# Performance work log

Measured on AMD Instinct MI355X. Metric: run time of the kernel, lower is better.

The kernel has to match this reference:

```python
import jax, jax.numpy as jnp
import numpy as np

B, N, E, F_IN, F_OUT, F_EDGE = 8, 1024, 1536, 64, 64, 32


def _build_graph(seed=0):
    rng = np.random.default_rng(seed)
    src = rng.integers(0, N, size=E)
    off = rng.integers(1, N, size=E)
    dst = (src + off) % N  # guaranteed distinct from src
    inc = np.zeros((N, E), dtype=np.float32)
    inc[src, np.arange(E)] = 1.0
    inc[dst, np.arange(E)] = 1.0
    adj = np.zeros((N, N), dtype=np.float32)
    adj[src, dst] = 1.0
    adj[dst, src] = 1.0
    adj_sl = adj + np.eye(N, dtype=np.float32)
    deg = adj_sl.sum(axis=1)
    dinv = (1.0 / np.sqrt(deg)).astype(np.float32)  # D^{-1/2}, diag
    lap = (dinv[:, None] * adj_sl * dinv[None, :]).astype(np.float32)
    return inc, lap


def setup_inputs() -> dict:
    key = jax.random.key(0)
    k1, k2, k3, k4 = jax.random.split(key, 4)
    inc, lap = _build_graph()
    return {
        "nodes": jax.random.normal(k1, (B, N, F_IN), dtype=jnp.float32),
        "edges": jax.random.normal(k2, (B, E, F_EDGE), dtype=jnp.float32),
        "weight_matrix": jax.random.normal(k3, (F_IN, F_OUT), dtype=jnp.float32),
        "edge_weight_vec": jax.random.normal(k4, (F_EDGE,), dtype=jnp.float32),
        "inc_matrix": jnp.asarray(inc),
        "norm_symm_laplacian": jnp.asarray(lap),
    }


def reference(nodes, edges, weight_matrix, edge_weight_vec, inc_matrix, norm_symm_laplacian):
    # edge feature reduction: [B,E,F_e] @ [F_e] -> [B,E]
    ew = jnp.einsum("bef,f->be", edges, edge_weight_vec)
    # TDT[b,i,j] = sum_e over edges incident to BOTH i and j of ew[b,e].
    # This replaces the original per-(i,j) Python-dict gather loop with one
    # fused contraction over the binary incidence mask.
    incb = (inc_matrix != 0).astype(ew.dtype)           # [N,E]
    tmp = incb[None, :, :] * ew[:, None, :]             # [B,N,E]
    tdt = jnp.einsum("bie,je->bij", tmp, incb)          # [B,N,N]
    a_mat = tdt * norm_symm_laplacian                   # elementwise with D^-1/2(A+I)D^-1/2
    h = nodes @ weight_matrix                           # [B,N,F_out]
    return jnp.einsum("bij,bjf->bif", a_mat, h)         # [B,N,F_out]
```

## Files before the change

### kernel.cpp

```cpp
#include <hip/hip_runtime.h>

#define B_ 8
#define N_ 1024
#define E_ 1536
#define FIN_ 64
#define FOUT_ 64
#define FEDGE_ 32

#define WS_CNT   0
#define WS_ENDS  6144
#define WS_EW    18432
#define WS_DIAG  67584
#define WS_H     100352
#define WS_ZERO_BYTES 100352

__global__ __launch_bounds__(256) void extract_edges(const float* __restrict__ inc,
                                                     int* __restrict__ cnt,
                                                     int* __restrict__ ends) {
    int e = blockIdx.x * 256 + threadIdx.x;
    int i = blockIdx.y;
    if (e >= E_) return;
    if (inc[(size_t)i * E_ + e] != 0.0f) {
        int p = atomicAdd(&cnt[e], 1);
        ends[e * 2 + p] = i;
    }
}

__global__ __launch_bounds__(256) void edge_weights(const float* __restrict__ edges,
                                                    const float* __restrict__ evec,
                                                    const int* __restrict__ ends,
                                                    float* __restrict__ ew,
                                                    float* __restrict__ diag) {
    int t = blockIdx.x * 256 + threadIdx.x;
    if (t >= B_ * E_) return;
    int b = t / E_;
    int e = t - b * E_;
    const float* ep = edges + (size_t)t * FEDGE_;
    float s = 0.0f;
#pragma unroll
    for (int f = 0; f < FEDGE_; ++f) s += ep[f] * evec[f];
    ew[t] = s;
    int u = ends[2 * e];
    int v = ends[2 * e + 1];
    atomicAdd(&diag[b * N_ + u], s);
    atomicAdd(&diag[b * N_ + v], s);
}

__global__ __launch_bounds__(256) void node_transform(const float* __restrict__ nodes,
                                                      const float* __restrict__ W,
                                                      float* __restrict__ h) {
    __shared__ float Wl[FIN_ * FOUT_];
    __shared__ float rows[4 * FIN_];
    int tid = threadIdx.x;
#pragma unroll
    for (int k = tid; k < FIN_ * FOUT_; k += 256) Wl[k] = W[k];
    int row0 = blockIdx.x * 4;
    rows[tid] = nodes[(size_t)row0 * FIN_ + tid];
    __syncthreads();
    int r = tid >> 6;
    int f = tid & 63;
    float acc = 0.0f;
#pragma unroll
    for (int k = 0; k < FIN_; ++k) acc += rows[r * FIN_ + k] * Wl[k * FOUT_ + f];
    h[(size_t)(row0 + r) * FOUT_ + f] = acc;
}

__global__ __launch_bounds__(256) void scatter_edges(const int* __restrict__ ends,
                                                     const float* __restrict__ ew,
                                                     const float* __restrict__ lap,
                                                     const float* __restrict__ h,
                                                     float* __restrict__ out) {
    int wave = (blockIdx.x * 256 + threadIdx.x) >> 6;
    int lane = threadIdx.x & 63;
    if (wave >= B_ * E_) return;
    int b = wave / E_;
    int e = wave - b * E_;
    int u = ends[2 * e];
    int v = ends[2 * e + 1];
    float s = ew[wave] * lap[(size_t)u * N_ + v];
    const float* hb = h + (size_t)b * N_ * FOUT_;
    float* ob = out + (size_t)b * N_ * FOUT_;
    float hv = hb[(size_t)v * FOUT_ + lane];
    float hu = hb[(size_t)u * FOUT_ + lane];
    atomicAdd(&ob[(size_t)u * FOUT_ + lane], s * hv);
    atomicAdd(&ob[(size_t)v * FOUT_ + lane], s * hu);
}

__global__ __launch_bounds__(256) void add_diag(const float* __restrict__ diag,
                                                const float* __restrict__ lap,
                                                const float* __restrict__ h,
                                                float* __restrict__ out) {
    int t = blockIdx.x * 256 + threadIdx.x;
    if (t >= B_ * N_ * FOUT_) return;
    int bi = t >> 6;
    int i = bi & (N_ - 1);
    out[t] += diag[bi] * lap[(size_t)i * N_ + i] * h[t];
}

extern "C" void kernel_launch(void* const* d_in, const int* in_sizes, int n_in,
                              void* d_out, int out_size, void* d_ws, size_t ws_size,
                              hipStream_t stream) {
    const float* nodes = (const float*)d_in[0];
    const float* edges = (const float*)d_in[1];
    const float* W     = (const float*)d_in[2];
    const float* evec  = (const float*)d_in[3];
    const float* inc   = (const float*)d_in[4];
    const float* lap   = (const float*)d_in[5];
    float* out = (float*)d_out;

    char* ws = (char*)d_ws;
    int*   cnt  = (int*)(ws + WS_CNT);
    int*   ends = (int*)(ws + WS_ENDS);
    float* ew   = (float*)(ws + WS_EW);
    float* diag = (float*)(ws + WS_DIAG);
    float* h    = (float*)(ws + WS_H);

    hipMemsetAsync(ws, 0, WS_ZERO_BYTES, stream);
    hipMemsetAsync(d_out, 0, (size_t)out_size * sizeof(float), stream);

    extract_edges<<<dim3((E_ + 255) / 256, N_), 256, 0, stream>>>(inc, cnt, ends);
    node_transform<<<(B_ * N_) / 4, 256, 0, stream>>>(nodes, W, h);
    edge_weights<<<(B_ * E_ + 255) / 256, 256, 0, stream>>>(edges, evec, ends, ew, diag);
    scatter_edges<<<(B_ * E_ * 64) / 256, 256, 0, stream>>>(ends, ew, lap, h, out);
    add_diag<<<(B_ * N_ * FOUT_) / 256, 256, 0, stream>>>(diag, lap, h, out);
}
```

Measured before the change: 97.10 us.

## Fuse prep kernels and fold diagonal term into edge scatter

Merges node transform, incidence extraction and edge-weight reduction into one block-partitioned kernel, and zeroes the output there instead of with a memset. The separate diagonal kernel and its atomics are removed by having each edge add its self-loop contribution s*lap_ii*h_i during the scatter. Edge endpoints are found with atomicMin/atomicMax over a 0xAA-filled buffer using float4 reads. This cuts launch count and passes over the data, at the cost of a few extra lap loads per edge wave.

```diff
diff --git a/kernel.cpp b/kernel.cpp
--- a/kernel.cpp
+++ b/kernel.cpp
@@ -7,94 +7,97 @@
 #define FOUT_ 64
 #define FEDGE_ 32
 
-#define WS_CNT   0
-#define WS_ENDS  6144
-#define WS_EW    18432
-#define WS_DIAG  67584
-#define WS_H     100352
-#define WS_ZERO_BYTES 100352
+#define WS_LO   0
+#define WS_HI   6144
+#define WS_EW   12288
+#define WS_H    61440
 
-__global__ __launch_bounds__(256) void extract_edges(const float* __restrict__ inc,
-                                                     int* __restrict__ cnt,
-                                                     int* __restrict__ ends) {
-    int e = blockIdx.x * 256 + threadIdx.x;
-    int i = blockIdx.y;
-    if (e >= E_) return;
-    if (inc[(size_t)i * E_ + e] != 0.0f) {
-        int p = atomicAdd(&cnt[e], 1);
-        ends[e * 2 + p] = i;
+#define NT_BLOCKS 2048
+#define EX_BLOCKS 1536
+#define EW_BLOCKS 48
+#define K1_BLOCKS (NT_BLOCKS + EX_BLOCKS + EW_BLOCKS)
+
+__global__ __launch_bounds__(256) void fused_prep(
+    const float* __restrict__ nodes,
+    const float* __restrict__ W,
+    const float* __restrict__ inc,
+    const float* __restrict__ edges,
+    const float* __restrict__ evec,
+    unsigned*    __restrict__ ends_lo,
+    int*         __restrict__ ends_hi,
+    float*       __restrict__ ew,
+    float*       __restrict__ h,
+    float*       __restrict__ out)
+{
+    __shared__ float Wl[FIN_ * FOUT_];
+    __shared__ float rows[4 * FIN_];
+    const int blk = blockIdx.x;
+    const int tid = threadIdx.x;
+
+    if (blk < NT_BLOCKS) {
+#pragma unroll
+        for (int k = tid; k < FIN_ * FOUT_; k += 256) Wl[k] = W[k];
+        const int row0 = blk * 4;
+        rows[tid] = nodes[(size_t)row0 * FIN_ + tid];
+        __syncthreads();
+        const int r = tid >> 6;
+        const int f = tid & 63;
+        float acc = 0.0f;
+#pragma unroll
+        for (int k = 0; k < FIN_; ++k) acc += rows[r * FIN_ + k] * Wl[k * FOUT_ + f];
+        const size_t o = (size_t)(row0 + r) * FOUT_ + f;
+        h[o] = acc;
+        out[o] = 0.0f;
+    } else if (blk < NT_BLOCKS + EX_BLOCKS) {
+        const int g = (blk - NT_BLOCKS) * 256 + tid;
+        const int row = g / (E_ / 4);
+        const int q = g - row * (E_ / 4);
+        const float4 c = ((const float4*)inc)[g];
+        const int e0 = q * 4;
+        if (c.x != 0.0f) { atomicMin(&ends_lo[e0 + 0], (unsigned)row); atomicMax(&ends_hi[e0 + 0], row); }
+        if (c.y != 0.0f) { atomicMin(&ends_lo[e0 + 1], (unsigned)row); atomicMax(&ends_hi[e0 + 1], row); }
+        if (c.z != 0.0f) { atomicMin(&ends_lo[e0 + 2], (unsigned)row); atomicMax(&ends_hi[e0 + 2], row); }
+        if (c.w != 0.0f) { atomicMin(&ends_lo[e0 + 3], (unsigned)row); atomicMax(&ends_hi[e0 + 3], row); }
+    } else {
+        const int t = (blk - NT_BLOCKS - EX_BLOCKS) * 256 + tid;
+        const float4* ep = (const float4*)(edges + (size_t)t * FEDGE_);
+        float s = 0.0f;
+#pragma unroll
+        for (int j = 0; j < FEDGE_ / 4; ++j) {
+            const float4 a = ep[j];
+            s += a.x * evec[4 * j + 0] + a.y * evec[4 * j + 1]
+               + a.z * evec[4 * j + 2] + a.w * evec[4 * j + 3];
+        }
+        ew[t] = s;
     }
 }
 
-__global__ __launch_bounds__(256) void edge_weights(const float* __restrict__ edges,
-                                                    const float* __restrict__ evec,
-                                                    const int* __restrict__ ends,
-                                                    float* __restrict__ ew,
-                                                    float* __restrict__ diag) {
-    int t = blockIdx.x * 256 + threadIdx.x;
-    if (t >= B_ * E_) return;
-    int b = t / E_;
-    int e = t - b * E_;
-    const float* ep = edges + (size_t)t * FEDGE_;
-    float s = 0.0f;
-#pragma unroll
-    for (int f = 0; f < FEDGE_; ++f) s += ep[f] * evec[f];
-    ew[t] = s;
-    int u = ends[2 * e];
-    int v = ends[2 * e + 1];
-    atomicAdd(&diag[b * N_ + u], s);
-    atomicAdd(&diag[b * N_ + v], s);
-}
-
-__global__ __launch_bounds__(256) void node_transform(const float* __restrict__ nodes,
-                                                      const float* __restrict__ W,
-                                                      float* __restrict__ h) {
-    __shared__ float Wl[FIN_ * FOUT_];
-    __shared__ float rows[4 * FIN_];
-    int tid = threadIdx.x;
-#pragma unroll
-    for (int k = tid; k < FIN_ * FOUT_; k += 256) Wl[k] = W[k];
-    int row0 = blockIdx.x * 4;
-    rows[tid] = nodes[(size_t)row0 * FIN_ + tid];
-    __syncthreads();
-    int r = tid >> 6;
-    int f = tid & 63;
-    float acc = 0.0f;
-#pragma unroll
-    for (int k = 0; k < FIN_; ++k) acc += rows[r * FIN_ + k] * Wl[k * FOUT_ + f];
-    h[(size_t)(row0 + r) * FOUT_ + f] = acc;
-}
-
-__global__ __launch_bounds__(256) void scatter_edges(const int* __restrict__ ends,
-                                                     const float* __restrict__ ew,
-                                                     const float* __restrict__ lap,
-                                                     const float* __restrict__ h,
-                                                     float* __restrict__ out) {
-    int wave = (blockIdx.x * 256 + threadIdx.x) >> 6;
-    int lane = threadIdx.x & 63;
-    if (wave >= B_ * E_) return;
-    int b = wave / E_;
-    int e = wave - b * E_;
-    int u = ends[2 * e];
-    int v = ends[2 * e + 1];
-    float s = ew[wave] * lap[(size_t)u * N_ + v];
+__global__ __launch_bounds__(256) void scatter_edges(
+    const unsigned* __restrict__ ends_lo,
+    const int*      __restrict__ ends_hi,
+    const float*    __restrict__ ew,
+    const float*    __restrict__ lap,
+    const float*    __restrict__ h,
+    float*          __restrict__ out)
+{
+    const int wid = (blockIdx.x * 256 + threadIdx.x) >> 6;
+    const int lane = threadIdx.x & 63;
+    if (wid >= B_ * E_) return;
+    const int b = wid / E_;
+    const int e = wid - b * E_;
+    const int u = (int)ends_lo[e];
+    const int v = ends_hi[e];
+    const float s = ew[wid];
+    const float* lrow = lap + (size_t)u * N_;
+    const float luv = lrow[v];
+    const float luu = lrow[u];
+    const float lvv = lap[(size_t)v * N_ + v];
     const float* hb = h + (size_t)b * N_ * FOUT_;
     float* ob = out + (size_t)b * N_ * FOUT_;
-    float hv = hb[(size_t)v * FOUT_ + lane];
-    float hu = hb[(size_t)u * FOUT_ + lane];
-    atomicAdd(&ob[(size_t)u * FOUT_ + lane], s * hv);
-    atomicAdd(&ob[(size_t)v * FOUT_ + lane], s * hu);
-}
-
-__global__ __launch_bounds__(256) void add_diag(const float* __restrict__ diag,
-                                                const float* __restrict__ lap,
-                                                const float* __restrict__ h,
-                                                float* __restrict__ out) {
-    int t = blockIdx.x * 256 + threadIdx.x;
-    if (t >= B_ * N_ * FOUT_) return;
-    int bi = t >> 6;
-    int i = bi & (N_ - 1);
-    out[t] += diag[bi] * lap[(size_t)i * N_ + i] * h[t];
+    const float hu = hb[(size_t)u * FOUT_ + lane];
+    const float hv = hb[(size_t)v * FOUT_ + lane];
+    atomicAdd(&ob[(size_t)u * FOUT_ + lane], s * (luv * hv + luu * hu));
+    atomicAdd(&ob[(size_t)v * FOUT_ + lane], s * (luv * hu + lvv * hv));
 }
 
 extern "C" void kernel_launch(void* const* d_in, const int* in_sizes, int n_in,
@@ -109,18 +112,14 @@
     float* out = (float*)d_out;
 
     char* ws = (char*)d_ws;
-    int*   cnt  = (int*)(ws + WS_CNT);
-    int*   ends = (int*)(ws + WS_ENDS);
-    float* ew   = (float*)(ws + WS_EW);
-    float* diag = (float*)(ws + WS_DIAG);
-    float* h    = (float*)(ws + WS_H);
+    unsigned* ends_lo = (unsigned*)(ws + WS_LO);
+    int*      ends_hi = (int*)(ws + WS_HI);
+    float*    ew      = (float*)(ws + WS_EW);
+    float*    h       = (float*)(ws + WS_H);
 
-    hipMemsetAsync(ws, 0, WS_ZERO_BYTES, stream);
-    hipMemsetAsync(d_out, 0, (size_t)out_size * sizeof(float), stream);
+    hipMemsetAsync(ws, 0xAA, 2 * E_ * sizeof(int), stream);
 
-    extract_edges<<<dim3((E_ + 255) / 256, N_), 256, 0, stream>>>(inc, cnt, ends);
-    node_transform<<<(B_ * N_) / 4, 256, 0, stream>>>(nodes, W, h);
-    edge_weights<<<(B_ * E_ + 255) / 256, 256, 0, stream>>>(edges, evec, ends, ew, diag);
-    scatter_edges<<<(B_ * E_ * 64) / 256, 256, 0, stream>>>(ends, ew, lap, h, out);
-    add_diag<<<(B_ * N_ * FOUT_) / 256, 256, 0, stream>>>(diag, lap, h, out);
+    fused_prep<<<K1_BLOCKS, 256, 0, stream>>>(nodes, W, inc, edges, evec,
+                                              ends_lo, ends_hi, ew, h, out);
+    scatter_edges<<<(B_ * E_ * 64) / 256, 256, 0, stream>>>(ends_lo, ends_hi, ew, lap, h, out);
 }
```

Measured after the change: 85.36 us. -12.1%, faster.
